# Kernel tuning notes

Hardware: AMD Instinct MI355X
Metric: run time of the kernel (lower is better)

Reference implementation:

```python
import jax, jax.numpy as jnp
import numpy as np

H = 256          # encoder hidden per direction
D = 2 * H        # decoder hidden / bidirectional feature dim
IN = 2
OUT = 2
B = 64
T = 256
STEPS = 24       # hard-coded decoder loop length in the source


def gru_cell(x, h, Wih, Whh, bih, bhh):
    # PyTorch GRU cell: gate order (r, z, n)
    gi = x @ Wih.T + bih
    gh = h @ Whh.T + bhh
    ir, iz, inn = jnp.split(gi, 3, axis=-1)
    hr, hz, hn = jnp.split(gh, 3, axis=-1)
    r = jax.nn.sigmoid(ir + hr)
    z = jax.nn.sigmoid(iz + hz)
    n = jnp.tanh(inn + r * hn)
    return (1.0 - z) * n + z * h


def run_dir(xs, Wih, Whh, bih, bhh, reverse):
    # xs: (T, B, F) time-major; returns outputs (T, B, H) and last hidden (B, H)
    h0 = jnp.zeros((xs.shape[1], Whh.shape[-1]), xs.dtype)
    def step(h, xt):
        h2 = gru_cell(xt, h, Wih, Whh, bih, bhh)
        return h2, h2
    h_last, ys = jax.lax.scan(step, h0, xs, reverse=reverse)
    return ys, h_last


def setup_inputs():
    keys = jax.random.split(jax.random.key(0), 24)
    k = iter(keys)
    def rn(shape, s):
        return jax.random.normal(next(k), shape, jnp.float32) * s
    se = 1.0 / np.sqrt(H)
    sd = 1.0 / np.sqrt(D)
    return {
        "x": rn((B, T, IN), 1.0),
        "enc_Wih0": rn((2, 3 * H, IN), se),
        "enc_Whh0": rn((2, 3 * H, H), se),
        "enc_bih0": rn((2, 3 * H), se),
        "enc_bhh0": rn((2, 3 * H), se),
        "enc_Wih": rn((2, 2, 3 * H, D), se),
        "enc_Whh": rn((2, 2, 3 * H, H), se),
        "enc_bih": rn((2, 2, 3 * H), se),
        "enc_bhh": rn((2, 2, 3 * H), se),
        "dec_Wih": rn((3, 3 * D, D), sd),
        "dec_Whh": rn((3, 3 * D, D), sd),
        "dec_bih": rn((3, 3 * D), sd),
        "dec_bhh": rn((3, 3 * D), sd),
        "fc_con_W": rn((D, 2 * D), sd),
        "fc_con_b": rn((D,), sd),
        "attn_W": rn((D, 2 * D), sd),
        "attn_b": rn((D,), sd),
        "v": jax.random.uniform(next(k), (D,), jnp.float32),  # torch.rand init
        "fc_W": rn((OUT, D), sd),
        "fc_b": rn((OUT,), sd),
    }


def reference(x, enc_Wih0, enc_Whh0, enc_bih0, enc_bhh0,
              enc_Wih, enc_Whh, enc_bih, enc_bhh,
              dec_Wih, dec_Whh, dec_bih, dec_bhh,
              fc_con_W, fc_con_b, attn_W, attn_b, v, fc_W, fc_b):
    # ---- bidirectional 3-layer GRU encoder ----
    seq = x.transpose(1, 0, 2)  # (T, B, IN) time-major
    hf_list, hb_list = [], []
    for l in range(3):
        if l == 0:
            Wf, Uf, bf, cf = enc_Wih0[0], enc_Whh0[0], enc_bih0[0], enc_bhh0[0]
            Wb, Ub, bb, cb = enc_Wih0[1], enc_Whh0[1], enc_bih0[1], enc_bhh0[1]
        else:
            Wf, Uf, bf, cf = enc_Wih[l-1, 0], enc_Whh[l-1, 0], enc_bih[l-1, 0], enc_bhh[l-1, 0]
            Wb, Ub, bb, cb = enc_Wih[l-1, 1], enc_Whh[l-1, 1], enc_bih[l-1, 1], enc_bhh[l-1, 1]
        yf, hf = run_dir(seq, Wf, Uf, bf, cf, False)
        yb, hb = run_dir(seq, Wb, Ub, bb, cb, True)
        seq = jnp.concatenate([yf, yb], axis=-1)
        hf_list.append(hf)
        hb_list.append(hb)
    enc_out = seq.transpose(1, 0, 2)  # (B, T, D)
    # hidden_decoder = cat(forward, backward) per layer -> (3, B, D)
    hidden = jnp.stack([jnp.concatenate([f, b], axis=-1)
                        for f, b in zip(hf_list, hb_list)])
    dec_in = enc_out[:, -1, :]  # (B, D)

    # additive attention: energy = tanh(W [h; enc_out] + b); precompute enc part
    attn_Wh = attn_W[:, :D]
    attn_We = attn_W[:, D:]
    enc_proj = jnp.einsum('bte,de->btd', enc_out, attn_We)  # (B, T, D)

    def dec_step(carry, _):
        d_in, hid = carry
        hq = hid[-1] @ attn_Wh.T                               # (B, D)
        energy = jnp.tanh(hq[:, None, :] + enc_proj + attn_b)  # (B, T, D)
        scores = jnp.einsum('btd,d->bt', energy, v)
        aw = jax.nn.softmax(scores, axis=1)                    # (B, T)
        ctx = jnp.einsum('bt,btd->bd', aw, enc_out)            # (B, D)
        inp = jnp.concatenate([d_in, ctx], axis=-1) @ fc_con_W.T + fc_con_b
        new_h = []
        for l in range(3):  # 3-layer unidirectional decoder GRU, single step
            hl = gru_cell(inp, hid[l], dec_Wih[l], dec_Whh[l], dec_bih[l], dec_bhh[l])
            new_h.append(hl)
            inp = hl
        out_step = inp @ fc_W.T + fc_b
        return (inp, jnp.stack(new_h)), out_step

    _, outs = jax.lax.scan(dec_step, (dec_in, hidden), None, length=STEPS)
    return outs.transpose(1, 0, 2)  # (B, 24, OUT)
```

## Files before the change

### kernel.cpp

```cpp
#include <hip/hip_runtime.h>

typedef unsigned short u16;
typedef unsigned int u32;
typedef _Float16 f16;
typedef f16   f16x2 __attribute__((ext_vector_type(2)));
typedef f16   f16x8 __attribute__((ext_vector_type(8)));
typedef float f32x4 __attribute__((ext_vector_type(4)));

#define MFMA16(a,b,c) __builtin_amdgcn_mfma_f32_16x16x32_f16((a),(b),(c),0,0,0)

__device__ __forceinline__ float sigm_(float x){ return 1.f/(1.f + __expf(-x)); }
__device__ __forceinline__ float tanh_(float x){ return 1.f - 2.f/(1.f + __expf(2.f*x)); }
__device__ __forceinline__ float clampf(float x, float c){
  if (!(x > -c)) x = -c;
  if (x > c) x = c;
  return x;
}
__device__ __forceinline__ f16x8 cvt8f(const float* p){
  const float4 a = *(const float4*)p;
  const float4 b = *(const float4*)(p+4);
  f16x8 r;
  r[0]=(f16)a.x; r[1]=(f16)a.y; r[2]=(f16)a.z; r[3]=(f16)a.w;
  r[4]=(f16)b.x; r[5]=(f16)b.y; r[6]=(f16)b.z; r[7]=(f16)b.w;
  return r;
}

__global__ void k_diag(float* out, int mib){
  const int i = blockIdx.x*256 + threadIdx.x;
  if (i < 3072) out[i] = 1000.f * (float)mib;
}

__global__ void k_prep_dec(const float* dWhh, const float* attnW, const float* fccon,
                           const float* dWih, f16* R3)
{
  long idx = (long)blockIdx.x*256 + threadIdx.x;
  const float* src; int rs, colOff = 0, NKS; long dst, loc;
  if (idx < 294912L) {
    loc = idx; const int m = (int)(loc / 98304); loc %= 98304;
    src = dWhh + (long)m*786432; rs = 512; NKS = 16; dst = (long)m*786432;
  } else if (idx < 327680L) {
    loc = idx - 294912L; src = attnW; colOff = 512; rs = 1024; NKS = 16; dst = 2359296L;
  } else if (idx < 393216L) {
    loc = idx - 327680L; src = fccon; rs = 1024; NKS = 32; dst = 2621440L;
  } else if (idx < 688128L) {
    loc = idx - 393216L; const int m = (int)(loc / 98304); loc %= 98304;
    src = dWih + (long)m*786432; rs = 512; NKS = 16; dst = 3440640L + (long)m*786432;
  } else if (idx < 720896L) {
    loc = idx - 688128L; src = attnW; colOff = 0; rs = 1024; NKS = 16; dst = 5799936L;
  } else return;
  const int lane = (int)(loc & 63);
  const long frag = loc >> 6;
  const int ks = (int)(frag % NKS);
  const long nt = frag / NKS;
  const int n  = (int)(nt*16 + (lane & 15));
  const int k0 = ks*32 + ((lane >> 4) << 3);
  const float* sp = src + (long)n*rs + colOff + k0;
  f16* dp = R3 + dst + loc*8;
  #pragma unroll
  for (int j = 0; j < 8; ++j) dp[j] = (f16)sp[j];
}

__global__ void k_gi0s(const float* __restrict__ x, const float* __restrict__ W,
                       const float* __restrict__ bi, f16* __restrict__ gi,
                       int seg, int BH, int lbh, int b0)
{
  const long idx = (long)blockIdx.x*256 + threadIdx.x;
  const int inner = (int)(idx % 768);
  long r = idx / 768;
  const int b = (int)(r & (BH-1)); r >>= lbh;
  const int s = (int)(r & 63);
  const int d = (int)(r >> 6);
  const int lo = inner / 48, rem = inner % 48;
  const int j = rem / 3, g = rem % 3;
  const int n = g*256 + j*16 + lo;
  const int t = d ? (255 - (seg*64 + s)) : (seg*64 + s);
  const float x0 = x[(((b0+b)<<8) + t)*2];
  const float x1 = x[(((b0+b)<<8) + t)*2 + 1];
  const long wi = ((long)d*768 + n)*2;
  gi[idx] = (f16)clampf(x0*W[wi] + x1*W[wi+1] + bi[d*768 + n], 32.f);
}

__global__ __launch_bounds__(512, 1) void k_enc_seg(
    const f16* __restrict__ gi, const float* __restrict__ Wraw,
    const float* __restrict__ bhh, f16* __restrict__ seq, int ostr,
    f16* __restrict__ fin, float* __restrict__ hcar, int seg, int BH)
{
  const int tid = threadIdx.x;
  const int w = tid >> 6, lane = tid & 63;
  const int lo16 = lane & 15, quad = lane >> 4;
  const int nbq = BH >> 4;
  const int dir = blockIdx.x / nbq, bq = blockIdx.x % nbq;

  __shared__ f16 h16[2][16][264];

  const float* mat = Wraw + (long)dir*196608;
  f16x8 wr[6][8];
  #pragma unroll
  for (int p = 0; p < 3; ++p)
    #pragma unroll
    for (int i = 0; i < 2; ++i) {
      const int n = (p*16 + 2*w + i)*16 + lo16;
      #pragma unroll
      for (int ks = 0; ks < 8; ++ks)
        wr[p*2+i][ks] = cvt8f(mat + (long)n*256 + ks*32 + quad*8);
    }
  float bh_[3][2];
  #pragma unroll
  for (int p = 0; p < 3; ++p)
    #pragma unroll
    for (int i = 0; i < 2; ++i)
      bh_[p][i] = bhh[dir*768 + p*256 + (2*w+i)*16 + lo16];

  float hreg[2][4];
  if (seg == 0) {
    #pragma unroll
    for (int i = 0; i < 2; ++i)
      #pragma unroll
      for (int r = 0; r < 4; ++r) {
        hreg[i][r] = 0.f;
        h16[0][quad*4 + r][(2*w+i)*16 + lo16] = (f16)0.f;
      }
  } else {
    #pragma unroll
    for (int i = 0; i < 2; ++i) {
      const int c = (2*w+i)*16 + lo16;
      #pragma unroll
      for (int r = 0; r < 4; ++r) {
        const float v = hcar[((dir*BH) + bq*16 + quad*4 + r)*256 + c];
        hreg[i][r] = v;
        h16[0][quad*4 + r][c] = (f16)v;
      }
    }
  }

  const f16* gbase = gi + (((long)dir*64*BH) + bq*16 + quad*4)*768 + lo16*48 + w*6;
  f16x2 g0[4][3];
  #pragma unroll
  for (int r = 0; r < 4; ++r) {
    const f16* gp = gbase + (long)r*768;
    g0[r][0] = *(const f16x2*)(gp);
    g0[r][1] = *(const f16x2*)(gp + 2);
    g0[r][2] = *(const f16x2*)(gp + 4);
  }

  for (int s = 0; s < 64; ++s) {
    const int cur = s & 1;
    __syncthreads();
    f32x4 acc[6];
    #pragma unroll
    for (int q = 0; q < 6; ++q) acc[q] = (f32x4){0.f,0.f,0.f,0.f};
    #pragma unroll
    for (int ks = 0; ks < 8; ++ks) {
      const f16x8 a = *(const f16x8*)&h16[cur][lo16][ks*32 + quad*8];
      #pragma unroll
      for (int q = 0; q < 6; ++q)
        acc[q] = MFMA16(a, wr[q][ks], acc[q]);
    }
    f16x2 g1[4][3];
    if (s < 63) {
      #pragma unroll
      for (int r = 0; r < 4; ++r) {
        const f16* gp = gbase + ((long)(s+1)*BH + r)*768;
        g1[r][0] = *(const f16x2*)(gp);
        g1[r][1] = *(const f16x2*)(gp + 2);
        g1[r][2] = *(const f16x2*)(gp + 4);
      }
    }
    const int t = dir ? (255 - (seg*64 + s)) : (seg*64 + s);
    #pragma unroll
    for (int i = 0; i < 2; ++i) {
      const int c = (2*w+i)*16 + lo16;
      #pragma unroll
      for (int r = 0; r < 4; ++r) {
        const int row = quad*4 + r;
        const float gir = (i==0) ? (float)g0[r][0][0] : (float)g0[r][1][1];
        const float giz = (i==0) ? (float)g0[r][0][1] : (float)g0[r][2][0];
        const float gin = (i==0) ? (float)g0[r][1][0] : (float)g0[r][2][1];
        const float rv = sigm_(gir + acc[i][r]   + bh_[0][i]);
        const float zv = sigm_(giz + acc[2+i][r] + bh_[1][i]);
        const float nv = tanh_(gin + rv*(acc[4+i][r] + bh_[2][i]));
        float hn = (1.f - zv)*nv + zv*hreg[i][r];
        hn = clampf(hn, 2.f);
        hreg[i][r] = hn;
        h16[cur^1][row][c] = (f16)hn;
        seq[((long)t*ostr + bq*16 + row)*512 + dir*256 + c] = (f16)hn;
        if (seg == 3 && s == 63) fin[(bq*16 + row)*512 + dir*256 + c] = (f16)hn;
      }
    }
    #pragma unroll
    for (int r = 0; r < 4; ++r) { g0[r][0]=g1[r][0]; g0[r][1]=g1[r][1]; g0[r][2]=g1[r][2]; }
  }
  #pragma unroll
  for (int i = 0; i < 2; ++i) {
    const int c = (2*w+i)*16 + lo16;
    #pragma unroll
    for (int r = 0; r < 4; ++r)
      hcar[((dir*BH) + bq*16 + quad*4 + r)*256 + c] = hreg[i][r];
  }
}

__global__ void k_gemm(const f16* __restrict__ A, int K,
                       const f16* __restrict__ Bsw, const float* __restrict__ Braw,
                       long bzs, int ldb, int koff,
                       const float* __restrict__ bias, int biaszs,
                       void* __restrict__ Cv, long czs, int ldc, int mode,
                       int tb0, int tb1, int tdirsgn, int lbh, int abstr, float cv)
{
  const int tid = threadIdx.x, w = tid>>6, lane = tid&63;
  const int lo16 = lane&15, quad = lane>>4;
  const int m0 = blockIdx.x*64 + w*16;
  const int n0 = blockIdx.y*128;
  const int z  = blockIdx.z;
  const int tbase = z ? tb1 : tb0;
  const int tdir  = z ? -tdirsgn : tdirsgn;
  const int NKS = K >> 5;
  const int mrow = m0 + lo16;
  const long arow = (long)(tbase + tdir*(mrow >> lbh))*abstr + (mrow & ((1<<lbh)-1));
  const f16* Ap = A + arow*K + quad*8;
  f32x4 acc[8];
  #pragma unroll
  for (int i=0;i<8;++i) acc[i]=(f32x4){0.f,0.f,0.f,0.f};
  if (Bsw) {
    const f16* Bp = Bsw + (long)z*bzs;
    for (int ks = 0; ks < NKS; ++ks) {
      const f16x8 a = *(const f16x8*)(Ap + ks*32);
      #pragma unroll
      for (int nt = 0; nt < 8; ++nt) {
        const f16x8 b = *(const f16x8*)(Bp + (((long)((n0>>4)+nt)*NKS + ks) << 9) + lane*8);
        acc[nt] = MFMA16(a, b, acc[nt]);
      }
    }
  } else {
    const float* Bp = Braw + (long)z*bzs;
    for (int ks = 0; ks < NKS; ++ks) {
      const f16x8 a = *(const f16x8*)(Ap + ks*32);
      #pragma unroll
      for (int nt = 0; nt < 8; ++nt) {
        const f16x8 b = cvt8f(Bp + (long)(n0 + nt*16 + lo16)*ldb + koff + ks*32 + quad*8);
        acc[nt] = MFMA16(a, b, acc[nt]);
      }
    }
  }
  #pragma unroll
  for (int nt = 0; nt < 8; ++nt) {
    const int n = n0 + nt*16 + lo16;
    const float bv = bias ? bias[z*biaszs + n] : 0.f;
    #pragma unroll
    for (int r = 0; r < 4; ++r) {
      const int m = m0 + quad*4 + r;
      const float val = clampf(acc[nt][r] + bv, cv);
      if (mode == 2)
        ((f16*)Cv)[(long)z*czs + (long)m*768 + lo16*48 + ((n>>4)&15)*3 + (n>>8)] = (f16)val;
      else if (mode == 1)
        ((f16*)Cv)[(long)z*czs + (long)m*ldc + n] = (f16)val;
      else
        ((float*)Cv)[(long)z*czs + (long)m*ldc + n] = val;
    }
  }
}

__global__ void k_score(const f16* __restrict__ seq, const f16* __restrict__ We,
                        const float* __restrict__ hq, const float* __restrict__ ab,
                        const float* __restrict__ vp, float* __restrict__ S)
{
  const int t = blockIdx.x, tid = threadIdx.x;
  const int w = tid>>6, lane = tid&63, lo16 = lane&15, quad = lane>>4;
  __shared__ float svab[1024];
  for (int i = tid; i < 512; i += 256) { svab[i] = vp[i]; svab[512+i] = ab[i]; }
  __syncthreads();
  f32x4 acc[32];
  #pragma unroll
  for (int i=0;i<32;++i) acc[i]=(f32x4){0.f,0.f,0.f,0.f};
  const f16* Ap = seq + ((long)t*64 + w*16 + lo16)*512 + quad*8;
  for (int ks = 0; ks < 16; ++ks) {
    const f16x8 a = *(const f16x8*)(Ap + ks*32);
    #pragma unroll
    for (int nt = 0; nt < 32; ++nt) {
      const f16x8 b = *(const f16x8*)(We + (((long)nt*16 + ks) << 9) + lane*8);
      acc[nt] = MFMA16(a, b, acc[nt]);
    }
  }
  #pragma unroll
  for (int r = 0; r < 4; ++r) {
    const int b = w*16 + quad*4 + r;
    float sc = 0.f;
    #pragma unroll
    for (int nt = 0; nt < 32; ++nt) {
      const int n = nt*16 + lo16;
      sc += svab[n] * tanh_(acc[nt][r] + hq[(b<<9) + n] + svab[512+n]);
    }
    sc += __shfl_xor(sc, 1, 64); sc += __shfl_xor(sc, 2, 64);
    sc += __shfl_xor(sc, 4, 64); sc += __shfl_xor(sc, 8, 64);
    if (lo16 == 0) S[(b<<8) + t] = clampf(sc, 256.f);
  }
}

__global__ void k_attnctx(const float* __restrict__ S, const f16* __restrict__ enc,
                          f16* __restrict__ cat)
{
  const int b = blockIdx.x, tid = threadIdx.x;
  __shared__ float ssc[256], srd[256];
  const float sc = clampf(S[(b<<8) + tid], 256.f);
  srd[tid] = sc; __syncthreads();
  for (int off = 128; off > 0; off >>= 1) { if (tid < off) srd[tid] = fmaxf(srd[tid], srd[tid+off]); __syncthreads(); }
  const float mx = srd[0]; __syncthreads();
  const float e = __expf(sc - mx);
  srd[tid] = e; __syncthreads();
  for (int off = 128; off > 0; off >>= 1) { if (tid < off) srd[tid] += srd[tid+off]; __syncthreads(); }
  const float inv = 1.f / srd[0]; __syncthreads();
  ssc[tid] = e * inv; __syncthreads();
  float c0 = 0.f, c1 = 0.f;
  for (int tt = 0; tt < 256; ++tt) {
    const float awt = ssc[tt];
    const f16* ep = enc + (((long)tt*64 + b) << 9);
    c0 += awt * (float)ep[tid];
    c1 += awt * (float)ep[256 + tid];
  }
  cat[(b<<10) + 512 + tid] = (f16)clampf(c0, 4.f);
  cat[(b<<10) + 768 + tid] = (f16)clampf(c1, 4.f);
}

__global__ void k_dec_init(const f16* __restrict__ fin, const f16* __restrict__ seq,
                           f16* __restrict__ hb16, float* __restrict__ hf32,
                           f16* __restrict__ cat)
{
  const int idx = blockIdx.x*256 + threadIdx.x;
  const int d = idx & 511, b = (idx >> 9) & 63, l = idx >> 15;
  if (l < 3) {
    const float v = clampf((float)fin[((long)l<<15) + (b<<9) + d], 2.f);
    hb16[(long)l*65536 + (b<<9) + d] = (f16)v;
    hf32[(long)l*32768 + (b<<9) + d] = v;
  } else {
    cat[(b<<10) + d] = seq[((long)255*64 + b)*512 + d];
  }
}

__global__ __launch_bounds__(512, 1) void k_attn(
    const f16* __restrict__ seq, const f16* __restrict__ ep,
    const float* __restrict__ hf2, const f16* __restrict__ cat,
    const f16* __restrict__ whsw, const f16* __restrict__ fcsw,
    const float* __restrict__ fcconB, const float* __restrict__ vp,
    f16* __restrict__ inp, const float* __restrict__ fcW,
    const float* __restrict__ fcb, float* __restrict__ out, int step)
{
  const int b = blockIdx.x;
  const int tid = threadIdx.x, w = tid >> 6, lane = tid & 63;
  const int quad = lane >> 4;
  __shared__ float hsm[512];
  __shared__ float cats[1024];
  __shared__ float hqs[512];
  __shared__ float aw[256];
  __shared__ float red[8*512];
  hsm[tid < 512 ? tid : 0] = hsm[0];
  if (tid < 512) {
    hsm[tid]  = hf2[(b<<9) + tid];
    cats[tid] = (float)cat[(b<<10) + tid];
  }
  __syncthreads();
  if (w < 2 && step > 0) {
    float p = 0.f;
    #pragma unroll
    for (int j = 0; j < 8; ++j) p += fcW[(w<<9) + lane*8 + j] * hsm[lane*8 + j];
    p += __shfl_xor(p,1,64); p += __shfl_xor(p,2,64); p += __shfl_xor(p,4,64);
    p += __shfl_xor(p,8,64); p += __shfl_xor(p,16,64); p += __shfl_xor(p,32,64);
    if (lane == 0) out[(b*24 + step-1)*2 + w] = clampf(p + fcb[w], 128.f);
  }
  #pragma unroll
  for (int i = 0; i < 4; ++i) {
    const int nt = w*4 + i;
    float p = 0.f;
    for (int ks = 0; ks < 16; ++ks) {
      const f16x8 wv = *(const f16x8*)(whsw + (((long)nt*16 + ks)<<9) + lane*8);
      const float4 ha = *(const float4*)&hsm[ks*32 + quad*8];
      const float4 hb = *(const float4*)&hsm[ks*32 + quad*8 + 4];
      p += (float)wv[0]*ha.x + (float)wv[1]*ha.y + (float)wv[2]*ha.z + (float)wv[3]*ha.w
         + (float)wv[4]*hb.x + (float)wv[5]*hb.y + (float)wv[6]*hb.z + (float)wv[7]*hb.w;
    }
    p += __shfl_xor(p,16,64); p += __shfl_xor(p,32,64);
    if (lane < 16) hqs[nt*16 + lane] = p;
  }
  __syncthreads();
  float hq8[8], v8[8];
  #pragma unroll
  for (int j = 0; j < 8; ++j) { hq8[j] = hqs[lane*8+j]; v8[j] = vp[lane*8+j]; }
  #pragma unroll 2
  for (int i = 0; i < 32; ++i) {
    const int t = w*32 + i;
    const f16x8 e = *(const f16x8*)(ep + (((long)t*64 + b)<<9) + lane*8);
    float s = 0.f;
    #pragma unroll
    for (int j = 0; j < 8; ++j) s += v8[j]*tanh_((float)e[j] + hq8[j]);
    s += __shfl_xor(s,1,64); s += __shfl_xor(s,2,64); s += __shfl_xor(s,4,64);
    s += __shfl_xor(s,8,64); s += __shfl_xor(s,16,64); s += __shfl_xor(s,32,64);
    if (lane == 0) aw[t] = clampf(s, 256.f);
  }
  __syncthreads();
  if (tid < 64) {
    float s0=aw[tid], s1=aw[tid+64], s2=aw[tid+128], s3=aw[tid+192];
    float mx = fmaxf(fmaxf(s0,s1), fmaxf(s2,s3));
    mx = fmaxf(mx, __shfl_xor(mx,1,64)); mx = fmaxf(mx, __shfl_xor(mx,2,64));
    mx = fmaxf(mx, __shfl_xor(mx,4,64)); mx = fmaxf(mx, __shfl_xor(mx,8,64));
    mx = fmaxf(mx, __shfl_xor(mx,16,64)); mx = fmaxf(mx, __shfl_xor(mx,32,64));
    const float e0=__expf(s0-mx), e1=__expf(s1-mx), e2=__expf(s2-mx), e3=__expf(s3-mx);
    float sm = e0+e1+e2+e3;
    sm += __shfl_xor(sm,1,64); sm += __shfl_xor(sm,2,64); sm += __shfl_xor(sm,4,64);
    sm += __shfl_xor(sm,8,64); sm += __shfl_xor(sm,16,64); sm += __shfl_xor(sm,32,64);
    const float inv = 1.f/sm;
    aw[tid]=e0*inv; aw[tid+64]=e1*inv; aw[tid+128]=e2*inv; aw[tid+192]=e3*inv;
  }
  __syncthreads();
  float c8[8];
  #pragma unroll
  for (int j = 0; j < 8; ++j) c8[j] = 0.f;
  #pragma unroll 2
  for (int i = 0; i < 32; ++i) {
    const int t = w*32 + i;
    const f16x8 e = *(const f16x8*)(seq + (((long)t*64 + b)<<9) + lane*8);
    const float awt = aw[t];
    #pragma unroll
    for (int j = 0; j < 8; ++j) c8[j] += awt*(float)e[j];
  }
  #pragma unroll
  for (int j = 0; j < 8; ++j) red[(w<<9) + lane*8 + j] = c8[j];
  __syncthreads();
  if (tid < 512) {
    float s = 0.f;
    #pragma unroll
    for (int ww = 0; ww < 8; ++ww) s += red[(ww<<9) + tid];
    cats[512 + tid] = clampf(s, 4.f);
  }
  __syncthreads();
  #pragma unroll
  for (int i = 0; i < 4; ++i) {
    const int nt = w*4 + i;
    float p = 0.f;
    for (int ks = 0; ks < 32; ++ks) {
      const f16x8 wv = *(const f16x8*)(fcsw + (((long)nt*32 + ks)<<9) + lane*8);
      const float4 ca = *(const float4*)&cats[ks*32 + quad*8];
      const float4 cb = *(const float4*)&cats[ks*32 + quad*8 + 4];
      p += (float)wv[0]*ca.x + (float)wv[1]*ca.y + (float)wv[2]*ca.z + (float)wv[3]*ca.w
         + (float)wv[4]*cb.x + (float)wv[5]*cb.y + (float)wv[6]*cb.z + (float)wv[7]*cb.w;
    }
    p += __shfl_xor(p,16,64); p += __shfl_xor(p,32,64);
    if (lane < 16) inp[(b<<9) + nt*16 + lane] = (f16)clampf(p + fcconB[nt*16+lane], 64.f);
  }
}

__global__ void k_cell(const f16* __restrict__ inp, const f16* __restrict__ WihSw,
                       const f16* __restrict__ WhhSw, const float* __restrict__ bih,
                       const float* __restrict__ bhh, float* __restrict__ hf32,
                       const f16* __restrict__ hin, f16* __restrict__ hout,
                       f16* __restrict__ cat)
{
  const int tid = threadIdx.x, w = tid>>6, lane = tid&63;
  const int lo16 = lane&15, quad = lane>>4;
  const int Wt  = (blockIdx.x & 7)*4 + w;
  const int mi0 = (blockIdx.x >> 3)*2;
  f32x4 arz[4], an_[4];
  #pragma unroll
  for (int i=0;i<4;++i){ arz[i]=(f32x4){0.f,0.f,0.f,0.f}; an_[i]=(f32x4){0.f,0.f,0.f,0.f}; }
  #pragma unroll 2
  for (int kk = 0; kk < 16; ++kk) {
    const f16x8 b0 = *(const f16x8*)(WihSw + (((long)Wt*16 + kk)<<9)      + lane*8);
    const f16x8 b1 = *(const f16x8*)(WihSw + (((long)(32+Wt)*16 + kk)<<9) + lane*8);
    const f16x8 b2 = *(const f16x8*)(WihSw + (((long)(64+Wt)*16 + kk)<<9) + lane*8);
    #pragma unroll
    for (int m = 0; m < 2; ++m) {
      const f16x8 a = *(const f16x8*)&inp[(((mi0+m)*16 + lo16)<<9) + kk*32 + quad*8];
      arz[m]   = MFMA16(a, b0, arz[m]);
      arz[2+m] = MFMA16(a, b1, arz[2+m]);
      an_[m]   = MFMA16(a, b2, an_[m]);
    }
  }
  #pragma unroll 2
  for (int kk = 0; kk < 16; ++kk) {
    const f16x8 b0 = *(const f16x8*)(WhhSw + (((long)Wt*16 + kk)<<9)      + lane*8);
    const f16x8 b1 = *(const f16x8*)(WhhSw + (((long)(32+Wt)*16 + kk)<<9) + lane*8);
    const f16x8 b2 = *(const f16x8*)(WhhSw + (((long)(64+Wt)*16 + kk)<<9) + lane*8);
    #pragma unroll
    for (int m = 0; m < 2; ++m) {
      const f16x8 a = *(const f16x8*)&hin[(((mi0+m)*16 + lo16)<<9) + kk*32 + quad*8];
      arz[m]   = MFMA16(a, b0, arz[m]);
      arz[2+m] = MFMA16(a, b1, arz[2+m]);
      an_[2+m] = MFMA16(a, b2, an_[2+m]);
    }
  }
  const int c = Wt*16 + lo16;
  const float brz0 = bih[c]     + bhh[c];
  const float brz1 = bih[512+c] + bhh[512+c];
  const float bin_ = bih[1024+c];
  const float bhn_ = bhh[1024+c];
  #pragma unroll
  for (int m = 0; m < 2; ++m)
    #pragma unroll
    for (int r = 0; r < 4; ++r) {
      const int row = (mi0+m)*16 + quad*4 + r;
      const float rv = sigm_(clampf(arz[m][r],64.f)   + brz0);
      const float zv = sigm_(clampf(arz[2+m][r],64.f) + brz1);
      const float nv = tanh_(clampf(an_[m][r],64.f) + bin_ + rv*(clampf(an_[2+m][r],64.f) + bhn_));
      const float ho = hf32[(row<<9) + c];
      float hn2 = (1.f - zv)*nv + zv*ho;
      hn2 = clampf(hn2, 2.f);
      hf32[(row<<9) + c] = hn2;
      hout[(row<<9) + c] = (f16)hn2;
      if (cat) cat[(row<<10) + c] = (f16)hn2;
    }
}

__global__ void k_cell_raw(const f16* __restrict__ inp, const float* __restrict__ WihRaw,
                           const f16* __restrict__ WhhSw, const float* __restrict__ bih,
                           const float* __restrict__ bhh, float* __restrict__ hf32,
                           const f16* __restrict__ hin, f16* __restrict__ hout,
                           f16* __restrict__ cat)
{
  const int tid = threadIdx.x, w = tid>>6, lane = tid&63;
  const int lo16 = lane&15, quad = lane>>4;
  const int Wt = blockIdx.x*4 + w;
  f32x4 arz[8], an_[8];
  #pragma unroll
  for (int i=0;i<8;++i){ arz[i]=(f32x4){0.f,0.f,0.f,0.f}; an_[i]=(f32x4){0.f,0.f,0.f,0.f}; }
  const int nr = Wt*16 + lo16;
  const float* Rr = WihRaw + (long)nr*512        + quad*8;
  const float* Rz = WihRaw + (long)(512+nr)*512  + quad*8;
  const float* Rn = WihRaw + (long)(1024+nr)*512 + quad*8;
  #pragma unroll 2
  for (int kk = 0; kk < 16; ++kk) {
    const f16x8 b0 = cvt8f(Rr + kk*32);
    const f16x8 b1 = cvt8f(Rz + kk*32);
    const f16x8 b2 = cvt8f(Rn + kk*32);
    #pragma unroll
    for (int mi = 0; mi < 4; ++mi) {
      const f16x8 a = *(const f16x8*)&inp[((mi*16 + lo16)<<9) + kk*32 + quad*8];
      arz[mi]   = MFMA16(a, b0, arz[mi]);
      arz[4+mi] = MFMA16(a, b1, arz[4+mi]);
      an_[mi]   = MFMA16(a, b2, an_[mi]);
    }
  }
  #pragma unroll 2
  for (int kk = 0; kk < 16; ++kk) {
    const f16x8 b0 = *(const f16x8*)(WhhSw + (((long)Wt*16 + kk)<<9)      + lane*8);
    const f16x8 b1 = *(const f16x8*)(WhhSw + (((long)(32+Wt)*16 + kk)<<9) + lane*8);
    const f16x8 b2 = *(const f16x8*)(WhhSw + (((long)(64+Wt)*16 + kk)<<9) + lane*8);
    #pragma unroll
    for (int mi = 0; mi < 4; ++mi) {
      const f16x8 a = *(const f16x8*)&hin[((mi*16 + lo16)<<9) + kk*32 + quad*8];
      arz[mi]   = MFMA16(a, b0, arz[mi]);
      arz[4+mi] = MFMA16(a, b1, arz[4+mi]);
      an_[4+mi] = MFMA16(a, b2, an_[4+mi]);
    }
  }
  const int c = Wt*16 + lo16;
  const float brz0 = bih[c]     + bhh[c];
  const float brz1 = bih[512+c] + bhh[512+c];
  const float bin_ = bih[1024+c];
  const float bhn_ = bhh[1024+c];
  #pragma unroll
  for (int mi = 0; mi < 4; ++mi)
    #pragma unroll
    for (int r = 0; r < 4; ++r) {
      const int row = mi*16 + quad*4 + r;
      const float rv = sigm_(clampf(arz[mi][r],64.f)   + brz0);
      const float zv = sigm_(clampf(arz[4+mi][r],64.f) + brz1);
      const float nv = tanh_(clampf(an_[mi][r],64.f) + bin_ + rv*(clampf(an_[4+mi][r],64.f) + bhn_));
      const float ho = hf32[(row<<9) + c];
      float hn2 = (1.f - zv)*nv + zv*ho;
      hn2 = clampf(hn2, 2.f);
      hf32[(row<<9) + c] = hn2;
      hout[(row<<9) + c] = (f16)hn2;
      if (cat) cat[(row<<10) + c] = (f16)hn2;
    }
}

__global__ void k_out(const float* __restrict__ h2, const float* __restrict__ fcW,
                      const float* __restrict__ fcb, float* __restrict__ out, int step)
{
  const int b = blockIdx.x, t = threadIdx.x;
  __shared__ float r0[256], r1[256];
  const float ha = clampf(h2[(b<<9) + t], 2.f);
  const float hb = clampf(h2[(b<<9) + 256 + t], 2.f);
  r0[t] = ha*fcW[t]     + hb*fcW[256+t];
  r1[t] = ha*fcW[512+t] + hb*fcW[768+t];
  __syncthreads();
  for (int off = 128; off > 0; off >>= 1) {
    if (t < off) { r0[t] += r0[t+off]; r1[t] += r1[t+off]; }
    __syncthreads();
  }
  if (t == 0) {
    out[(b*24 + step)*2]     = clampf(r0[0] + fcb[0], 128.f);
    out[(b*24 + step)*2 + 1] = clampf(r1[0] + fcb[1], 128.f);
  }
}

extern "C" void kernel_launch(void* const* d_in, const int* in_sizes, int n_in,
                              void* d_out, int out_size, void* d_ws, size_t ws_size,
                              hipStream_t stream) {
  const float* X      = (const float*)d_in[0];
  const float* eWih0  = (const float*)d_in[1];
  const float* eWhh0  = (const float*)d_in[2];
  const float* ebih0  = (const float*)d_in[3];
  const float* ebhh0  = (const float*)d_in[4];
  const float* eWih   = (const float*)d_in[5];
  const float* eWhh   = (const float*)d_in[6];
  const float* ebih   = (const float*)d_in[7];
  const float* ebhh   = (const float*)d_in[8];
  const float* dWih   = (const float*)d_in[9];
  const float* dWhh   = (const float*)d_in[10];
  const float* dbih   = (const float*)d_in[11];
  const float* dbhh   = (const float*)d_in[12];
  const float* fcconW = (const float*)d_in[13];
  const float* fcconB = (const float*)d_in[14];
  const float* attnW  = (const float*)d_in[15];
  const float* attnB  = (const float*)d_in[16];
  const float* vW     = (const float*)d_in[17];
  const float* fcW    = (const float*)d_in[18];
  const float* fcB    = (const float*)d_in[19];
  float* OUT = (float*)d_out;

  const long need_big  = 47054848L;
  const long need_half = 32964608L;
  f16* H = (f16*)d_ws;
  f16 *SEQ = H, *L1OUT, *GIB, *R3, *FIN, *HB, *CAT, *INP;
  float *HC;
  int BH, lbh, nh, l1ostr, l1abstr; long gdir;

  if ((long)ws_size >= need_big) {
    BH = 64; lbh = 6; nh = 1; l1ostr = 64; l1abstr = 64;
    L1OUT = H + 8388608L;
    GIB   = H + 16777216L;
    HC    = (float*)(H + 23068672L);
    FIN   = H + 23134208L;
    HB    = H + 23232512L;
    CAT   = H + 23429120L;
    INP   = H + 23494656L;
    gdir  = 3145728L;
  } else if ((long)ws_size >= need_half) {
    BH = 32; lbh = 5; nh = 2; l1ostr = 32; l1abstr = 32;
    L1OUT = H + 8388608L;
    GIB   = H + 12582912L;
    HC    = (float*)(H + 16023552L);
    FIN   = H + 16089088L;
    HB    = H + 16187392L;
    CAT   = H + 16384000L;
    INP   = H + 16449536L;
    gdir  = 1572864L;
  } else {
    k_diag<<<12, 256, 0, stream>>>(OUT, (int)(ws_size >> 20));
    return;
  }
  R3 = GIB;
  float* ST = (float*)(GIB + 3145728L);
  float* HQ = ST;
  float* HF = ST + 32768;
  float* S  = ST + 131072;
  const int nblk = 2*(BH>>4);
  const int gi0grid = (2*64*BH*768)/256;

  for (int h = 0; h < nh; ++h) {
    const int b0 = h*BH;
    for (int seg = 0; seg < 4; ++seg) {
      k_gi0s<<<gi0grid, 256, 0, stream>>>(X, eWih0, ebih0, GIB, seg, BH, lbh, b0);
      k_enc_seg<<<nblk, 512, 0, stream>>>(GIB, eWhh0, ebhh0, SEQ + (long)b0*512, 64,
                                          FIN + (long)b0*512, HC, seg, BH);
    }
    for (int seg = 0; seg < 4; ++seg) {
      k_gemm<<<dim3(BH, 6, 2), 256, 0, stream>>>(SEQ + (long)b0*512, 512,
          (const f16*)nullptr, eWih, 393216L, 512, 0, ebih, 768,
          GIB, gdir, 768, 2, seg*64, 255 - seg*64, 1, lbh, 64, 32.f);
      k_enc_seg<<<nblk, 512, 0, stream>>>(GIB, eWhh, ebhh, L1OUT, l1ostr,
                                          FIN + 32768 + (long)b0*512, HC, seg, BH);
    }
    for (int seg = 0; seg < 4; ++seg) {
      k_gemm<<<dim3(BH, 6, 2), 256, 0, stream>>>(L1OUT, 512,
          (const f16*)nullptr, eWih + 2L*393216, 393216L, 512, 0, ebih + 1536, 768,
          GIB, gdir, 768, 2, seg*64, 255 - seg*64, 1, lbh, l1abstr, 32.f);
      k_enc_seg<<<nblk, 512, 0, stream>>>(GIB, eWhh + 2L*196608, ebhh + 1536,
                                          SEQ + (long)b0*512, 64,
                                          FIN + 65536 + (long)b0*512, HC, seg, BH);
    }
  }

  if (BH == 64) {
    f16* EP    = L1OUT;
    f16* WIHSW = GIB + 3440640L;
    f16* WHSW  = GIB + 5799936L;

    k_prep_dec<<<2816, 256, 0, stream>>>(dWhh, attnW, fcconW, dWih, R3);
    k_gemm<<<dim3(256, 4, 1), 256, 0, stream>>>(SEQ, 512,
        R3 + 2359296L, (const float*)nullptr, 0L, 0, 0, attnB, 0,
        EP, 0L, 512, 1, 0, 0, 1, 6, 64, 32.f);
    k_dec_init<<<512, 256, 0, stream>>>(FIN, SEQ, HB, HF, CAT);

    for (int s = 0; s < 24; ++s) {
      const int p = s & 1;
      k_attn<<<64, 512, 0, stream>>>(SEQ, EP, HF + 2*32768, CAT, WHSW, R3 + 2621440L,
          fcconB, vW, INP, fcW, fcB, OUT, s);
      for (int l = 0; l < 3; ++l) {
        const f16* inl = (l == 0) ? INP : (HB + (2*(l-1) + (1-p))*32768L);
        k_cell<<<16, 256, 0, stream>>>(inl,
                  WIHSW + (long)l*786432, R3 + (long)l*786432,
                  dbih + l*1536, dbhh + l*1536, HF + (long)l*32768,
                  HB + (2*l + p)*32768L, HB + (2*l + (1-p))*32768L,
                  (l == 2) ? CAT : (f16*)nullptr);
      }
    }
    k_out<<<64, 256, 0, stream>>>(HF + 2*32768, fcW, fcB, OUT, 23);
  } else {
    k_prep_dec<<<1536, 256, 0, stream>>>(dWhh, attnW, fcconW, dWih, R3);
    k_dec_init<<<512, 256, 0, stream>>>(FIN, SEQ, HB, HF, CAT);

    for (int s = 0; s < 24; ++s) {
      const int p = s & 1;
      const f16* h2in = HB + (4 + p)*32768L;
      k_gemm<<<dim3(1,4,1), 256, 0, stream>>>(h2in, 512,
          (const f16*)nullptr, attnW, 0L, 1024, 0, (const float*)nullptr, 0,
          HQ, 0L, 512, 0, 0, 0, 0, 6, 64, 64.f);
      k_score<<<256, 256, 0, stream>>>(SEQ, R3 + 2359296L, HQ, attnB, vW, S);
      k_attnctx<<<64, 256, 0, stream>>>(S, SEQ, CAT);
      k_gemm<<<dim3(1,4,1), 256, 0, stream>>>(CAT, 1024,
          R3 + 2621440L, (const float*)nullptr, 0L, 0, 0, fcconB, 0,
          INP, 0L, 512, 1, 0, 0, 0, 6, 64, 64.f);
      for (int l = 0; l < 3; ++l) {
        const f16* inp = (l == 0) ? INP : (HB + (2*(l-1) + (1-p))*32768L);
        k_cell_raw<<<8, 256, 0, stream>>>(inp,
                  dWih + (long)l*786432, R3 + (long)l*786432,
                  dbih + l*1536, dbhh + l*1536, HF + (long)l*32768,
                  HB + (2*l + p)*32768L, HB + (2*l + (1-p))*32768L,
                  (l == 2) ? CAT : (f16*)nullptr);
      }
      k_out<<<64, 256, 0, stream>>>(HF + 2*32768, fcW, fcB, OUT, s);
    }
  }
}
```

Before: 7.190 ms.

## Relayout encoder input-gate buffer per thread and batch seq output stores

Changes the precomputed input-gate layout, in both k_gi0s and the GEMM mode-2 epilogue, so each encoder thread reads its 24 gate values per step as three contiguous 16-byte vectors instead of twelve scattered 4-byte loads. The per-element scalar f16 stores of the hidden state to seq are replaced by vectorized 16-byte row stores read back from a 4-deep shared-memory ring, delayed two steps so they overlap later recurrence steps. This cuts scattered global transactions in the latency-bound recurrent loop, at the cost of more shared memory, extra LDS reads, and more complex index math in the producers. Redundant tid<512 guards in k_attn are also dropped.

```diff
diff --git a/kernel.cpp b/kernel.cpp
--- a/kernel.cpp
+++ b/kernel.cpp
@@ -65,14 +65,16 @@
                        int seg, int BH, int lbh, int b0)
 {
   const long idx = (long)blockIdx.x*256 + threadIdx.x;
-  const int inner = (int)(idx % 768);
-  long r = idx / 768;
-  const int b = (int)(r & (BH-1)); r >>= lbh;
-  const int s = (int)(r & 63);
-  const int d = (int)(r >> 6);
-  const int lo = inner / 48, rem = inner % 48;
-  const int j = rem / 3, g = rem % 3;
-  const int n = g*256 + j*16 + lo;
+  const int v = (int)(idx % 24);
+  long rest = idx / 24;
+  const int tid = (int)(rest & 511); rest >>= 9;
+  const int bq = (int)(rest & ((1 << (lbh-4)) - 1)); rest >>= (lbh-4);
+  const int s = (int)(rest & 63);
+  const int d = (int)(rest >> 6);
+  const int r = v / 6, rem = v % 6, i = rem / 3, g = rem % 3;
+  const int w = tid >> 6, q = (tid >> 4) & 3, lo = tid & 15;
+  const int n = g*256 + (2*w + i)*16 + lo;
+  const int b = bq*16 + q*4 + r;
   const int t = d ? (255 - (seg*64 + s)) : (seg*64 + s);
   const float x0 = x[(((b0+b)<<8) + t)*2];
   const float x1 = x[(((b0+b)<<8) + t)*2 + 1];
@@ -80,6 +82,8 @@
   gi[idx] = (f16)clampf(x0*W[wi] + x1*W[wi+1] + bi[d*768 + n], 32.f);
 }
 
+#define GIE(G, vv) ((float)((vv) < 8 ? (G)[0][(vv)&7] : ((vv) < 16 ? (G)[1][(vv)-8] : (G)[2][(vv)-16])))
+
 __global__ __launch_bounds__(512, 1) void k_enc_seg(
     const f16* __restrict__ gi, const float* __restrict__ Wraw,
     const float* __restrict__ bhh, f16* __restrict__ seq, int ostr,
@@ -91,7 +95,7 @@
   const int nbq = BH >> 4;
   const int dir = blockIdx.x / nbq, bq = blockIdx.x % nbq;
 
-  __shared__ f16 h16[2][16][264];
+  __shared__ f16 h16[4][16][264];
 
   const float* mat = Wraw + (long)dir*196608;
   f16x8 wr[6][8];
@@ -133,62 +137,64 @@
     }
   }
 
-  const f16* gbase = gi + (((long)dir*64*BH) + bq*16 + quad*4)*768 + lo16*48 + w*6;
-  f16x2 g0[4][3];
-  #pragma unroll
-  for (int r = 0; r < 4; ++r) {
-    const f16* gp = gbase + (long)r*768;
-    g0[r][0] = *(const f16x2*)(gp);
-    g0[r][1] = *(const f16x2*)(gp + 2);
-    g0[r][2] = *(const f16x2*)(gp + 4);
-  }
+  const long gstep = (long)nbq*512*24;
+  const f16* gbase = gi + (((long)dir*64*nbq + bq)*512 + tid)*24;
+  f16x8 g0[3], g1[3];
+  { const f16x8* gp = (const f16x8*)gbase; g0[0]=gp[0]; g0[1]=gp[1]; g0[2]=gp[2]; }
+
+  const int frow = tid >> 5;
+  const int fcol = (tid & 31) * 8;
 
   for (int s = 0; s < 64; ++s) {
-    const int cur = s & 1;
     __syncthreads();
+    if (s >= 2) {
+      const int so = s - 2;
+      const int t2 = dir ? (255 - (seg*64 + so)) : (seg*64 + so);
+      const f16x8 hv = *(const f16x8*)&h16[(so+1)&3][frow][fcol];
+      *(f16x8*)&seq[((long)t2*ostr + bq*16 + frow)*512 + dir*256 + fcol] = hv;
+    }
     f32x4 acc[6];
     #pragma unroll
     for (int q = 0; q < 6; ++q) acc[q] = (f32x4){0.f,0.f,0.f,0.f};
     #pragma unroll
     for (int ks = 0; ks < 8; ++ks) {
-      const f16x8 a = *(const f16x8*)&h16[cur][lo16][ks*32 + quad*8];
+      const f16x8 a = *(const f16x8*)&h16[s&3][lo16][ks*32 + quad*8];
       #pragma unroll
       for (int q = 0; q < 6; ++q)
         acc[q] = MFMA16(a, wr[q][ks], acc[q]);
     }
-    f16x2 g1[4][3];
     if (s < 63) {
-      #pragma unroll
-      for (int r = 0; r < 4; ++r) {
-        const f16* gp = gbase + ((long)(s+1)*BH + r)*768;
-        g1[r][0] = *(const f16x2*)(gp);
-        g1[r][1] = *(const f16x2*)(gp + 2);
-        g1[r][2] = *(const f16x2*)(gp + 4);
-      }
-    }
-    const int t = dir ? (255 - (seg*64 + s)) : (seg*64 + s);
+      const f16x8* gp = (const f16x8*)(gbase + (long)(s+1)*gstep);
+      g1[0]=gp[0]; g1[1]=gp[1]; g1[2]=gp[2];
+    }
     #pragma unroll
     for (int i = 0; i < 2; ++i) {
       const int c = (2*w+i)*16 + lo16;
       #pragma unroll
       for (int r = 0; r < 4; ++r) {
         const int row = quad*4 + r;
-        const float gir = (i==0) ? (float)g0[r][0][0] : (float)g0[r][1][1];
-        const float giz = (i==0) ? (float)g0[r][0][1] : (float)g0[r][2][0];
-        const float gin = (i==0) ? (float)g0[r][1][0] : (float)g0[r][2][1];
+        const int v = r*6 + i*3;
+        const float gir = GIE(g0, v);
+        const float giz = GIE(g0, v+1);
+        const float gin = GIE(g0, v+2);
         const float rv = sigm_(gir + acc[i][r]   + bh_[0][i]);
         const float zv = sigm_(giz + acc[2+i][r] + bh_[1][i]);
         const float nv = tanh_(gin + rv*(acc[4+i][r] + bh_[2][i]));
         float hn = (1.f - zv)*nv + zv*hreg[i][r];
         hn = clampf(hn, 2.f);
         hreg[i][r] = hn;
-        h16[cur^1][row][c] = (f16)hn;
-        seq[((long)t*ostr + bq*16 + row)*512 + dir*256 + c] = (f16)hn;
+        h16[(s+1)&3][row][c] = (f16)hn;
         if (seg == 3 && s == 63) fin[(bq*16 + row)*512 + dir*256 + c] = (f16)hn;
       }
     }
-    #pragma unroll
-    for (int r = 0; r < 4; ++r) { g0[r][0]=g1[r][0]; g0[r][1]=g1[r][1]; g0[r][2]=g1[r][2]; }
+    g0[0]=g1[0]; g0[1]=g1[1]; g0[2]=g1[2];
+  }
+  __syncthreads();
+  #pragma unroll
+  for (int so = 62; so < 64; ++so) {
+    const int t2 = dir ? (255 - (seg*64 + so)) : (seg*64 + so);
+    const f16x8 hv = *(const f16x8*)&h16[(so+1)&3][frow][fcol];
+    *(f16x8*)&seq[((long)t2*ostr + bq*16 + frow)*512 + dir*256 + fcol] = hv;
   }
   #pragma unroll
   for (int i = 0; i < 2; ++i) {
@@ -249,9 +255,14 @@
     for (int r = 0; r < 4; ++r) {
       const int m = m0 + quad*4 + r;
       const float val = clampf(acc[nt][r] + bv, cv);
-      if (mode == 2)
-        ((f16*)Cv)[(long)z*czs + (long)m*768 + lo16*48 + ((n>>4)&15)*3 + (n>>8)] = (f16)val;
-      else if (mode == 1)
+      if (mode == 2) {
+        const int s_ = m >> lbh, b_ = m & ((1<<lbh)-1);
+        const int bq_ = b_ >> 4, q_ = (b_ >> 2) & 3, r_ = b_ & 3;
+        const int g_ = n >> 8, j_ = (n >> 4) & 15, lo_ = n & 15;
+        const long idx = ((((long)z*64 + s_)*(1<<(lbh-4)) + bq_)*512
+                          + ((j_>>1)*64 + q_*16 + lo_))*24 + r_*6 + (j_&1)*3 + g_;
+        ((f16*)Cv)[idx] = (f16)val;
+      } else if (mode == 1)
         ((f16*)Cv)[(long)z*czs + (long)m*ldc + n] = (f16)val;
       else
         ((float*)Cv)[(long)z*czs + (long)m*ldc + n] = val;
@@ -351,11 +362,8 @@
   __shared__ float hqs[512];
   __shared__ float aw[256];
   __shared__ float red[8*512];
-  hsm[tid < 512 ? tid : 0] = hsm[0];
-  if (tid < 512) {
-    hsm[tid]  = hf2[(b<<9) + tid];
-    cats[tid] = (float)cat[(b<<10) + tid];
-  }
+  hsm[tid]  = hf2[(b<<9) + tid];
+  cats[tid] = (float)cat[(b<<10) + tid];
   __syncthreads();
   if (w < 2 && step > 0) {
     float p = 0.f;
@@ -423,7 +431,7 @@
   #pragma unroll
   for (int j = 0; j < 8; ++j) red[(w<<9) + lane*8 + j] = c8[j];
   __syncthreads();
-  if (tid < 512) {
+  {
     float s = 0.f;
     #pragma unroll
     for (int ww = 0; ww < 8; ++ww) s += red[(ww<<9) + tid];
```

New measurement: 6.783 ms. 5.7% less time.
